# Performance work log

Measured on AMD Instinct MI355X. Metric: run time of the kernel, lower is better.

## Reference

```python
import jax, jax.numpy as jnp
import numpy as np

N_COL, N_CON, E = 100000, 20000, 800000
D_COL, D_CON, H = 16, 8, 128


def _segment_mean(msgs, dst_idx, n_dst):
    # sum then divide by in-degree (0-degree nodes get 0, matching PyG scatter-mean)
    s = jax.ops.segment_sum(msgs, dst_idx, num_segments=n_dst)
    cnt = jax.ops.segment_sum(jnp.ones((dst_idx.shape[0], 1), msgs.dtype), dst_idx, num_segments=n_dst)
    return s / jnp.maximum(cnt, 1.0)


def _sage(x_src, x_dst, src_idx, dst_idx, Wl, bl, Wr):
    # PyG SAGEConv(mean): lin_l(mean_j x_j) + lin_r(x_i); lin_r has no bias
    agg = _segment_mean(x_src[src_idx], dst_idx, x_dst.shape[0])
    return agg @ Wl.T + bl + x_dst @ Wr.T


def setup_inputs():
    key = jax.random.key(0)
    ks = jax.random.split(key, 24)
    rn = lambda k, shape, s=0.05: jax.random.normal(k, shape, jnp.float32) * s
    z = lambda shape: jnp.zeros(shape, jnp.float32)
    inp = {
        'x_col': jax.random.normal(ks[0], (N_COL, D_COL), jnp.float32),
        'x_con': jax.random.normal(ks[1], (N_CON, D_CON), jnp.float32),
        'edge_col': jax.random.randint(ks[2], (E,), 0, N_COL, jnp.int32),
        'edge_con': jax.random.randint(ks[3], (E,), 0, N_CON, jnp.int32),
        'W_col': rn(ks[4], (H, D_COL)), 'b_col': z((H,)),
        'W_con': rn(ks[5], (H, D_CON)), 'b_con': z((H,)),
        'c1_cn_Wl': rn(ks[6], (H, H)), 'c1_cn_bl': z((H,)), 'c1_cn_Wr': rn(ks[7], (H, H)),
        'c1_nc_Wl': rn(ks[8], (H, H)), 'c1_nc_bl': z((H,)), 'c1_nc_Wr': rn(ks[9], (H, H)),
        'c2_cn_Wl': rn(ks[10], (H, H)), 'c2_cn_bl': z((H,)), 'c2_cn_Wr': rn(ks[11], (H, H)),
        'c2_nc_Wl': rn(ks[12], (H, H)), 'c2_nc_bl': z((H,)), 'c2_nc_Wr': rn(ks[13], (H, H)),
        'q_W1': rn(ks[14], (H // 2, H)), 'q_b1': z((H // 2,)),
        'q_W2': rn(ks[15], (1, H // 2)), 'q_b2': z((1,)),
    }
    return inp


def reference(x_col, x_con, edge_col, edge_con,
              W_col, b_col, W_con, b_con,
              c1_cn_Wl, c1_cn_bl, c1_cn_Wr, c1_nc_Wl, c1_nc_bl, c1_nc_Wr,
              c2_cn_Wl, c2_cn_bl, c2_cn_Wr, c2_nc_Wl, c2_nc_bl, c2_nc_Wr,
              q_W1, q_b1, q_W2, q_b2):
    relu = jax.nn.relu
    h_col = relu(x_col @ W_col.T + b_col)  # [N_COL, H]
    h_con = relu(x_con @ W_con.T + b_con)  # [N_CON, H]
    # conv1: 'serves' col->con, 'served_by' con->col (reverse edges)
    n_con = relu(_sage(h_col, h_con, edge_col, edge_con, c1_cn_Wl, c1_cn_bl, c1_cn_Wr))
    n_col = relu(_sage(h_con, h_col, edge_con, edge_col, c1_nc_Wl, c1_nc_bl, c1_nc_Wr))
    # conv2
    h_con2 = relu(_sage(n_col, n_con, edge_col, edge_con, c2_cn_Wl, c2_cn_bl, c2_cn_Wr))
    h_col2 = relu(_sage(n_con, n_col, edge_con, edge_col, c2_nc_Wl, c2_nc_bl, c2_nc_Wr))
    del h_con2  # constraint embeddings unused for Q-head
    q = relu(h_col2 @ q_W1.T + q_b1) @ q_W2.T + q_b2  # [N_COL, 1]
    return q[:, 0]
```

## Files before the change

### kernel.cpp

```cpp
#include <hip/hip_runtime.h>

#define N_COL 100000
#define N_CON 20000
#define HDIM 128
#define SCAN_B 1024

__global__ void transpose_k(const float* __restrict__ src, float* __restrict__ dst, int R, int C) {
    int idx = blockIdx.x * blockDim.x + threadIdx.x;
    if (idx < R * C) {
        int r = idx / C, c = idx - r * C;
        dst[c * R + r] = src[idx];
    }
}

template <int D>
__global__ __launch_bounds__(256) void encoder_k(const float* __restrict__ x,
                                                 const float* __restrict__ WT,
                                                 const float* __restrict__ b,
                                                 float* __restrict__ out, int N) {
    int idx = blockIdx.x * blockDim.x + threadIdx.x;
    if (idx >= N * HDIM) return;
    int n = idx >> 7, h = idx & 127;
    const float* xr = x + (size_t)n * D;
    float acc = b[h];
#pragma unroll
    for (int k = 0; k < D; k++) acc = fmaf(xr[k], WT[k * HDIM + h], acc);
    out[idx] = fmaxf(acc, 0.f);
}

__global__ void count_k(const int* __restrict__ ecol, const int* __restrict__ econ,
                        int* cnt_col, int* cnt_con, int E) {
    int e = blockIdx.x * blockDim.x + threadIdx.x;
    if (e < E) {
        atomicAdd(&cnt_col[ecol[e]], 1);
        atomicAdd(&cnt_con[econ[e]], 1);
    }
}

__global__ __launch_bounds__(256) void scan1_k(const int* __restrict__ cnt, int n,
                                               int* __restrict__ offs, int* __restrict__ partials) {
    __shared__ int lds[256];
    int t = threadIdx.x;
    int base = blockIdx.x * SCAN_B + t * 4;
    int v[4], s = 0;
#pragma unroll
    for (int i = 0; i < 4; i++) { int idx = base + i; v[i] = (idx < n) ? cnt[idx] : 0; s += v[i]; }
    lds[t] = s; __syncthreads();
    for (int off = 1; off < 256; off <<= 1) {
        int x = (t >= off) ? lds[t - off] : 0; __syncthreads();
        lds[t] += x; __syncthreads();
    }
    int excl = lds[t] - s;
    if (t == 255) partials[blockIdx.x] = lds[255];
    int run = excl;
#pragma unroll
    for (int i = 0; i < 4; i++) { int idx = base + i; if (idx < n) offs[idx] = run; run += v[i]; }
}

__global__ __launch_bounds__(256) void scan2_k(int* partials, int nb) {
    __shared__ int lds[256];
    int t = threadIdx.x;
    int v = (t < nb) ? partials[t] : 0;
    lds[t] = v; __syncthreads();
    for (int off = 1; off < 256; off <<= 1) {
        int x = (t >= off) ? lds[t - off] : 0; __syncthreads();
        lds[t] += x; __syncthreads();
    }
    if (t < nb) partials[t] = lds[t] - v;
}

__global__ void scan3_k(int* offs, int n, const int* __restrict__ partials) {
    int i = blockIdx.x * blockDim.x + threadIdx.x;
    if (i < n) offs[i] += partials[i / SCAN_B];
}

__global__ void fill_k(const int* __restrict__ sidx, const int* __restrict__ didx,
                       const int* __restrict__ offs, int* cursor, int* __restrict__ srclist, int E) {
    int e = blockIdx.x * blockDim.x + threadIdx.x;
    if (e < E) {
        int d = didx[e];
        int p = offs[d] + atomicAdd(&cursor[d], 1);
        srclist[p] = sidx[e];
    }
}

__global__ __launch_bounds__(256) void gather_mean_k(const float* __restrict__ tab,
                                                     const int* __restrict__ srclist,
                                                     const int* __restrict__ offs,
                                                     const int* __restrict__ cnt,
                                                     float* __restrict__ out, int N) {
    int wid = threadIdx.x >> 6, lane = threadIdx.x & 63;
    int n = blockIdx.x * 4 + wid;
    if (n >= N) return;
    int c = cnt[n], st = offs[n];
    const int* sl = srclist + st;
    int half = lane >> 5, q = (lane & 31) * 4;
    float ax = 0.f, ay = 0.f, az = 0.f, aw = 0.f;
    int j = 0;
    for (; j + 1 < c; j += 2) {
        int s = sl[j + half];
        float4 a = *reinterpret_cast<const float4*>(tab + (size_t)s * HDIM + q);
        ax += a.x; ay += a.y; az += a.z; aw += a.w;
    }
    if (j < c && half == 0) {
        int s = sl[j];
        float4 a = *reinterpret_cast<const float4*>(tab + (size_t)s * HDIM + q);
        ax += a.x; ay += a.y; az += a.z; aw += a.w;
    }
    ax += __shfl_xor(ax, 32); ay += __shfl_xor(ay, 32);
    az += __shfl_xor(az, 32); aw += __shfl_xor(aw, 32);
    if (half == 0) {
        float inv = 1.f / fmaxf((float)c, 1.f);
        float4 r; r.x = ax * inv; r.y = ay * inv; r.z = az * inv; r.w = aw * inv;
        *reinterpret_cast<float4*>(out + (size_t)n * HDIM + q) = r;
    }
}

__device__ __forceinline__ void gemm_core(float (*As)[36], float (*Ws)[132],
                                          const float* __restrict__ src,
                                          const float* __restrict__ W,
                                          int n0, int N, int t, float acc[4][8]) {
    int tx = t & 15, ty = t >> 4;
    int ar = t >> 2, akq = (t & 3) * 8;
    int wk = t >> 3, wc = (t & 7) * 16;
    for (int kb = 0; kb < 4; ++kb) {
        int k0 = kb * 32;
        {
            int row = n0 + ar;
            float4 v0 = make_float4(0.f, 0.f, 0.f, 0.f), v1 = v0;
            if (row < N) {
                const float* ap = src + (size_t)row * HDIM + k0 + akq;
                v0 = *reinterpret_cast<const float4*>(ap);
                v1 = *reinterpret_cast<const float4*>(ap + 4);
            }
            *reinterpret_cast<float4*>(&As[ar][akq]) = v0;
            *reinterpret_cast<float4*>(&As[ar][akq + 4]) = v1;
        }
        {
            const float* wp = W + (size_t)(k0 + wk) * HDIM + wc;
#pragma unroll
            for (int jj = 0; jj < 4; jj++)
                *reinterpret_cast<float4*>(&Ws[wk][wc + 4 * jj]) =
                    *reinterpret_cast<const float4*>(wp + 4 * jj);
        }
        __syncthreads();
#pragma unroll
        for (int k4 = 0; k4 < 8; ++k4) {
            float4 av[4];
#pragma unroll
            for (int i = 0; i < 4; i++)
                av[i] = *reinterpret_cast<const float4*>(&As[ty * 4 + i][k4 * 4]);
#pragma unroll
            for (int kk = 0; kk < 4; kk++) {
                float4 w0 = *reinterpret_cast<const float4*>(&Ws[k4 * 4 + kk][tx * 4]);
                float4 w1 = *reinterpret_cast<const float4*>(&Ws[k4 * 4 + kk][64 + tx * 4]);
                float w[8] = {w0.x, w0.y, w0.z, w0.w, w1.x, w1.y, w1.z, w1.w};
#pragma unroll
                for (int i = 0; i < 4; i++) {
                    float avk = (kk == 0) ? av[i].x : (kk == 1) ? av[i].y
                                : (kk == 2) ? av[i].z : av[i].w;
#pragma unroll
                    for (int j = 0; j < 8; j++) acc[i][j] = fmaf(avk, w[j], acc[i][j]);
                }
            }
        }
        __syncthreads();
    }
}

__global__ __launch_bounds__(256) void lin_k(const float* __restrict__ src,
                                             const float* __restrict__ WT,
                                             float* __restrict__ out, int N) {
    __shared__ __align__(16) float As[64][36];
    __shared__ __align__(16) float Ws[32][132];
    int t = threadIdx.x;
    int tx = t & 15, ty = t >> 4;
    int n0 = blockIdx.x * 64;
    float acc[4][8];
#pragma unroll
    for (int i = 0; i < 4; i++)
#pragma unroll
        for (int j = 0; j < 8; j++) acc[i][j] = 0.f;
    gemm_core(As, Ws, src, WT, n0, N, t, acc);
#pragma unroll
    for (int i = 0; i < 4; i++) {
        int row = n0 + ty * 4 + i;
        if (row < N) {
            float* op = out + (size_t)row * HDIM;
            *reinterpret_cast<float4*>(op + tx * 4) = make_float4(acc[i][0], acc[i][1], acc[i][2], acc[i][3]);
            *reinterpret_cast<float4*>(op + 64 + tx * 4) = make_float4(acc[i][4], acc[i][5], acc[i][6], acc[i][7]);
        }
    }
}

__global__ __launch_bounds__(256) void sage_gemm_k(const float* __restrict__ agg,
                                                   const float* __restrict__ xdst,
                                                   const float* __restrict__ WlT,
                                                   const float* __restrict__ bl,
                                                   const float* __restrict__ WrT,
                                                   float* __restrict__ out, int N) {
    __shared__ __align__(16) float As[64][36];
    __shared__ __align__(16) float Ws[32][132];
    int t = threadIdx.x;
    int tx = t & 15, ty = t >> 4;
    int n0 = blockIdx.x * 64;
    float acc[4][8];
#pragma unroll
    for (int i = 0; i < 4; i++)
#pragma unroll
        for (int j = 0; j < 8; j++) acc[i][j] = 0.f;
    gemm_core(As, Ws, agg, WlT, n0, N, t, acc);
    gemm_core(As, Ws, xdst, WrT, n0, N, t, acc);
    float4 b0 = *reinterpret_cast<const float4*>(bl + tx * 4);
    float4 b1 = *reinterpret_cast<const float4*>(bl + 64 + tx * 4);
    float bb[8] = {b0.x, b0.y, b0.z, b0.w, b1.x, b1.y, b1.z, b1.w};
#pragma unroll
    for (int i = 0; i < 4; i++) {
        int row = n0 + ty * 4 + i;
        if (row < N) {
            float4 r0, r1;
            r0.x = fmaxf(acc[i][0] + bb[0], 0.f);
            r0.y = fmaxf(acc[i][1] + bb[1], 0.f);
            r0.z = fmaxf(acc[i][2] + bb[2], 0.f);
            r0.w = fmaxf(acc[i][3] + bb[3], 0.f);
            r1.x = fmaxf(acc[i][4] + bb[4], 0.f);
            r1.y = fmaxf(acc[i][5] + bb[5], 0.f);
            r1.z = fmaxf(acc[i][6] + bb[6], 0.f);
            r1.w = fmaxf(acc[i][7] + bb[7], 0.f);
            float* op = out + (size_t)row * HDIM;
            *reinterpret_cast<float4*>(op + tx * 4) = r0;
            *reinterpret_cast<float4*>(op + 64 + tx * 4) = r1;
        }
    }
}

__global__ __launch_bounds__(256) void sage_add_k(const float* __restrict__ c0,
                                                  const float* __restrict__ xdst,
                                                  const float* __restrict__ WrT,
                                                  const float* __restrict__ bl,
                                                  float* __restrict__ out, int N) {
    __shared__ __align__(16) float As[64][36];
    __shared__ __align__(16) float Ws[32][132];
    int t = threadIdx.x;
    int tx = t & 15, ty = t >> 4;
    int n0 = blockIdx.x * 64;
    float acc[4][8];
#pragma unroll
    for (int i = 0; i < 4; i++)
#pragma unroll
        for (int j = 0; j < 8; j++) acc[i][j] = 0.f;
    gemm_core(As, Ws, xdst, WrT, n0, N, t, acc);
    float4 b0 = *reinterpret_cast<const float4*>(bl + tx * 4);
    float4 b1 = *reinterpret_cast<const float4*>(bl + 64 + tx * 4);
    float bb[8] = {b0.x, b0.y, b0.z, b0.w, b1.x, b1.y, b1.z, b1.w};
#pragma unroll
    for (int i = 0; i < 4; i++) {
        int row = n0 + ty * 4 + i;
        if (row < N) {
            const float* cp = c0 + (size_t)row * HDIM;
            float4 c0a = *reinterpret_cast<const float4*>(cp + tx * 4);
            float4 c0b = *reinterpret_cast<const float4*>(cp + 64 + tx * 4);
            float4 r0, r1;
            r0.x = fmaxf(acc[i][0] + c0a.x + bb[0], 0.f);
            r0.y = fmaxf(acc[i][1] + c0a.y + bb[1], 0.f);
            r0.z = fmaxf(acc[i][2] + c0a.z + bb[2], 0.f);
            r0.w = fmaxf(acc[i][3] + c0a.w + bb[3], 0.f);
            r1.x = fmaxf(acc[i][4] + c0b.x + bb[4], 0.f);
            r1.y = fmaxf(acc[i][5] + c0b.y + bb[5], 0.f);
            r1.z = fmaxf(acc[i][6] + c0b.z + bb[6], 0.f);
            r1.w = fmaxf(acc[i][7] + c0b.w + bb[7], 0.f);
            float* op = out + (size_t)row * HDIM;
            *reinterpret_cast<float4*>(op + tx * 4) = r0;
            *reinterpret_cast<float4*>(op + 64 + tx * 4) = r1;
        }
    }
}

__global__ __launch_bounds__(256) void sage_add_q_k(const float* __restrict__ c0,
                                                    const float* __restrict__ xdst,
                                                    const float* __restrict__ WrT,
                                                    const float* __restrict__ bl,
                                                    const float* __restrict__ W1T,
                                                    const float* __restrict__ b1v,
                                                    const float* __restrict__ W2,
                                                    const float* __restrict__ b2,
                                                    float* __restrict__ out, int N) {
    __shared__ __align__(16) char smem[33792];
    float (*As)[36] = reinterpret_cast<float(*)[36]>(smem);
    float (*Ws)[132] = reinterpret_cast<float(*)[132]>(smem + 9216);
    float (*H2)[132] = reinterpret_cast<float(*)[132]>(smem);
    int t = threadIdx.x;
    int tx = t & 15, ty = t >> 4;
    int n0 = blockIdx.x * 64;
    float acc[4][8];
#pragma unroll
    for (int i = 0; i < 4; i++)
#pragma unroll
        for (int j = 0; j < 8; j++) acc[i][j] = 0.f;
    gemm_core(As, Ws, xdst, WrT, n0, N, t, acc);
    {
        float4 b0 = *reinterpret_cast<const float4*>(bl + tx * 4);
        float4 b1 = *reinterpret_cast<const float4*>(bl + 64 + tx * 4);
        float bb[8] = {b0.x, b0.y, b0.z, b0.w, b1.x, b1.y, b1.z, b1.w};
#pragma unroll
        for (int i = 0; i < 4; i++) {
            int row = n0 + ty * 4 + i;
            float4 c0a = make_float4(0.f, 0.f, 0.f, 0.f), c0b = c0a;
            if (row < N) {
                const float* cp = c0 + (size_t)row * HDIM;
                c0a = *reinterpret_cast<const float4*>(cp + tx * 4);
                c0b = *reinterpret_cast<const float4*>(cp + 64 + tx * 4);
            }
            float4 r0, r1;
            r0.x = fmaxf(acc[i][0] + c0a.x + bb[0], 0.f);
            r0.y = fmaxf(acc[i][1] + c0a.y + bb[1], 0.f);
            r0.z = fmaxf(acc[i][2] + c0a.z + bb[2], 0.f);
            r0.w = fmaxf(acc[i][3] + c0a.w + bb[3], 0.f);
            r1.x = fmaxf(acc[i][4] + c0b.x + bb[4], 0.f);
            r1.y = fmaxf(acc[i][5] + c0b.y + bb[5], 0.f);
            r1.z = fmaxf(acc[i][6] + c0b.z + bb[6], 0.f);
            r1.w = fmaxf(acc[i][7] + c0b.w + bb[7], 0.f);
            float* hp = &H2[ty * 4 + i][0];
            *reinterpret_cast<float4*>(hp + tx * 4) = r0;
            *reinterpret_cast<float4*>(hp + 64 + tx * 4) = r1;
        }
    }
    __syncthreads();
    int tx2 = t & 7, ty2 = t >> 3;
    float acc2[2][8];
#pragma unroll
    for (int i = 0; i < 2; i++)
#pragma unroll
        for (int j = 0; j < 8; j++) acc2[i][j] = 0.f;
    for (int k4 = 0; k4 < HDIM / 4; ++k4) {
        float4 a0 = *reinterpret_cast<const float4*>(&H2[ty2 * 2 + 0][k4 * 4]);
        float4 a1 = *reinterpret_cast<const float4*>(&H2[ty2 * 2 + 1][k4 * 4]);
        float a[2][4] = {{a0.x, a0.y, a0.z, a0.w}, {a1.x, a1.y, a1.z, a1.w}};
#pragma unroll
        for (int kk = 0; kk < 4; kk++) {
            const float* wp = W1T + (size_t)(k4 * 4 + kk) * 64 + tx2 * 8;
            float4 w0 = *reinterpret_cast<const float4*>(wp);
            float4 w1 = *reinterpret_cast<const float4*>(wp + 4);
            float w[8] = {w0.x, w0.y, w0.z, w0.w, w1.x, w1.y, w1.z, w1.w};
#pragma unroll
            for (int i = 0; i < 2; i++)
#pragma unroll
                for (int j = 0; j < 8; j++) acc2[i][j] = fmaf(a[i][kk], w[j], acc2[i][j]);
        }
    }
    {
        float4 c0v = *reinterpret_cast<const float4*>(b1v + tx2 * 8);
        float4 c1v = *reinterpret_cast<const float4*>(b1v + tx2 * 8 + 4);
        float bb1[8] = {c0v.x, c0v.y, c0v.z, c0v.w, c1v.x, c1v.y, c1v.z, c1v.w};
        float4 d0 = *reinterpret_cast<const float4*>(W2 + tx2 * 8);
        float4 d1 = *reinterpret_cast<const float4*>(W2 + tx2 * 8 + 4);
        float w2[8] = {d0.x, d0.y, d0.z, d0.w, d1.x, d1.y, d1.z, d1.w};
#pragma unroll
        for (int i = 0; i < 2; i++) {
            float v = 0.f;
#pragma unroll
            for (int j = 0; j < 8; j++) v = fmaf(fmaxf(acc2[i][j] + bb1[j], 0.f), w2[j], v);
            v += __shfl_xor(v, 1);
            v += __shfl_xor(v, 2);
            v += __shfl_xor(v, 4);
            int row = n0 + ty2 * 2 + i;
            if (tx2 == 0 && row < N) out[row] = v + b2[0];
        }
    }
}

extern "C" void kernel_launch(void* const* d_in, const int* in_sizes, int n_in,
                              void* d_out, int out_size, void* d_ws, size_t ws_size,
                              hipStream_t stream) {
    const float* x_col = (const float*)d_in[0];
    const float* x_con = (const float*)d_in[1];
    const int* edge_col = (const int*)d_in[2];
    const int* edge_con = (const int*)d_in[3];
    const float* W_col = (const float*)d_in[4];
    const float* b_col = (const float*)d_in[5];
    const float* W_con = (const float*)d_in[6];
    const float* b_con = (const float*)d_in[7];
    const float* c1_cn_Wl = (const float*)d_in[8];
    const float* c1_cn_bl = (const float*)d_in[9];
    const float* c1_cn_Wr = (const float*)d_in[10];
    const float* c1_nc_Wl = (const float*)d_in[11];
    const float* c1_nc_bl = (const float*)d_in[12];
    const float* c1_nc_Wr = (const float*)d_in[13];
    const float* c2_nc_Wl = (const float*)d_in[17];
    const float* c2_nc_bl = (const float*)d_in[18];
    const float* c2_nc_Wr = (const float*)d_in[19];
    const float* q_W1 = (const float*)d_in[20];
    const float* q_b1 = (const float*)d_in[21];
    const float* q_W2 = (const float*)d_in[22];
    const float* q_b2 = (const float*)d_in[23];
    float* out = (float*)d_out;
    const int E = in_sizes[2];

    float* ws = (float*)d_ws;
    size_t o = 0;
    float* h_col = ws + o;   o += (size_t)N_COL * HDIM;
    float* h_con = ws + o;   o += (size_t)N_CON * HDIM;
    float* n_con = ws + o;   o += (size_t)N_CON * HDIM;
    float* n_col = ws + o;   o += (size_t)N_COL * HDIM;
    float* bufA = ws + o;    o += (size_t)N_COL * HDIM;
    float* bufB = ws + o;    o += (size_t)N_CON * HDIM;
    float* W_colT = ws + o;  o += 16 * HDIM;
    float* W_conT = ws + o;  o += 8 * HDIM;
    float* c1_cn_WlT = ws + o; o += HDIM * HDIM;
    float* c1_cn_WrT = ws + o; o += HDIM * HDIM;
    float* c1_nc_WlT = ws + o; o += HDIM * HDIM;
    float* c1_nc_WrT = ws + o; o += HDIM * HDIM;
    float* c2_nc_WlT = ws + o; o += HDIM * HDIM;
    float* c2_nc_WrT = ws + o; o += HDIM * HDIM;
    float* q_W1T = ws + o;     o += HDIM * 64;
    int* iws = (int*)(ws + o);
    size_t io = 0;
    int* cnt_col = iws + io;  io += N_COL;
    int* cnt_con = iws + io;  io += N_CON;
    int* offs_col = iws + io; io += N_COL;
    int* offs_con = iws + io; io += N_CON;
    int* cursor = iws + io;   io += N_COL;
    int* partials = iws + io; io += 256;
    int* srclist_col = iws + io; io += E;
    int* srclist_con = iws + io; io += E;

    auto T = [&](const float* s, float* d, int R, int C) {
        transpose_k<<<(R * C + 255) / 256, 256, 0, stream>>>(s, d, R, C);
    };
    T(W_col, W_colT, HDIM, 16);
    T(W_con, W_conT, HDIM, 8);
    T(c1_cn_Wl, c1_cn_WlT, HDIM, HDIM);
    T(c1_cn_Wr, c1_cn_WrT, HDIM, HDIM);
    T(c1_nc_Wl, c1_nc_WlT, HDIM, HDIM);
    T(c1_nc_Wr, c1_nc_WrT, HDIM, HDIM);
    T(c2_nc_Wl, c2_nc_WlT, HDIM, HDIM);
    T(c2_nc_Wr, c2_nc_WrT, HDIM, HDIM);
    T(q_W1, q_W1T, 64, HDIM);

    encoder_k<16><<<((size_t)N_COL * HDIM + 255) / 256, 256, 0, stream>>>(x_col, W_colT, b_col, h_col, N_COL);
    encoder_k<8><<<((size_t)N_CON * HDIM + 255) / 256, 256, 0, stream>>>(x_con, W_conT, b_con, h_con, N_CON);

    hipMemsetAsync(cnt_col, 0, (N_COL + N_CON) * sizeof(int), stream);
    count_k<<<(E + 255) / 256, 256, 0, stream>>>(edge_col, edge_con, cnt_col, cnt_con, E);

    int nb_col = (N_COL + SCAN_B - 1) / SCAN_B;
    int nb_con = (N_CON + SCAN_B - 1) / SCAN_B;
    scan1_k<<<nb_col, 256, 0, stream>>>(cnt_col, N_COL, offs_col, partials);
    scan2_k<<<1, 256, 0, stream>>>(partials, nb_col);
    scan3_k<<<(N_COL + 255) / 256, 256, 0, stream>>>(offs_col, N_COL, partials);
    scan1_k<<<nb_con, 256, 0, stream>>>(cnt_con, N_CON, offs_con, partials);
    scan2_k<<<1, 256, 0, stream>>>(partials, nb_con);
    scan3_k<<<(N_CON + 255) / 256, 256, 0, stream>>>(offs_con, N_CON, partials);

    hipMemsetAsync(cursor, 0, N_COL * sizeof(int), stream);
    fill_k<<<(E + 255) / 256, 256, 0, stream>>>(edge_con, edge_col, offs_col, cursor, srclist_col, E);
    hipMemsetAsync(cursor, 0, N_CON * sizeof(int), stream);
    fill_k<<<(E + 255) / 256, 256, 0, stream>>>(edge_col, edge_con, offs_con, cursor, srclist_con, E);

    gather_mean_k<<<(N_CON + 3) / 4, 256, 0, stream>>>(h_col, srclist_con, offs_con, cnt_con, bufA, N_CON);
    sage_gemm_k<<<(N_CON + 63) / 64, 256, 0, stream>>>(bufA, h_con, c1_cn_WlT, c1_cn_bl, c1_cn_WrT, n_con, N_CON);

    lin_k<<<(N_CON + 63) / 64, 256, 0, stream>>>(h_con, c1_nc_WlT, bufB, N_CON);
    gather_mean_k<<<(N_COL + 3) / 4, 256, 0, stream>>>(bufB, srclist_col, offs_col, cnt_col, bufA, N_COL);
    sage_add_k<<<(N_COL + 63) / 64, 256, 0, stream>>>(bufA, h_col, c1_nc_WrT, c1_nc_bl, n_col, N_COL);

    lin_k<<<(N_CON + 63) / 64, 256, 0, stream>>>(n_con, c2_nc_WlT, bufB, N_CON);
    gather_mean_k<<<(N_COL + 3) / 4, 256, 0, stream>>>(bufB, srclist_col, offs_col, cnt_col, bufA, N_COL);
    sage_add_q_k<<<(N_COL + 63) / 64, 256, 0, stream>>>(bufA, n_col, c2_nc_WrT, c2_nc_bl,
                                                        q_W1T, q_b1, q_W2, q_b2, out, N_COL);
}
```

Measured before the change: 743.3 us.

## Fuse both column SAGE layers and Q-head into one kernel keeping n_col in LDS

Both neighbour aggregations for column nodes now run before a single fused kernel. That kernel computes the conv1 column output tile, keeps it in shared memory, then applies the conv2 root-weight GEMM and the Q-head MLP on it. This is possible because the conv2 neighbour term depends only on n_con. It removes the global write and read of the 100000x128 n_col tensor and one kernel launch. In exchange, shared memory per block grows to about 59 KB, which may reduce occupancy, and the two aggregate buffers are kept in memory at the same time.

Result: slower. 763.1 us (+2.7%).

```diff
diff --git a/kernel.cpp b/kernel.cpp
--- a/kernel.cpp
+++ b/kernel.cpp
@@ -168,6 +168,45 @@
     }
 }
 
+__device__ __forceinline__ void gemm_core_h(float (*Ha)[132], float (*Ws)[132],
+                                            const float* __restrict__ W,
+                                            int t, float acc[4][8]) {
+    int tx = t & 15, ty = t >> 4;
+    int wk = t >> 3, wc = (t & 7) * 16;
+    for (int kb = 0; kb < 4; ++kb) {
+        int k0 = kb * 32;
+        {
+            const float* wp = W + (size_t)(k0 + wk) * HDIM + wc;
+#pragma unroll
+            for (int jj = 0; jj < 4; jj++)
+                *reinterpret_cast<float4*>(&Ws[wk][wc + 4 * jj]) =
+                    *reinterpret_cast<const float4*>(wp + 4 * jj);
+        }
+        __syncthreads();
+#pragma unroll
+        for (int k4 = 0; k4 < 8; ++k4) {
+            float4 av[4];
+#pragma unroll
+            for (int i = 0; i < 4; i++)
+                av[i] = *reinterpret_cast<const float4*>(&Ha[ty * 4 + i][k0 + k4 * 4]);
+#pragma unroll
+            for (int kk = 0; kk < 4; kk++) {
+                float4 w0 = *reinterpret_cast<const float4*>(&Ws[k4 * 4 + kk][tx * 4]);
+                float4 w1 = *reinterpret_cast<const float4*>(&Ws[k4 * 4 + kk][64 + tx * 4]);
+                float w[8] = {w0.x, w0.y, w0.z, w0.w, w1.x, w1.y, w1.z, w1.w};
+#pragma unroll
+                for (int i = 0; i < 4; i++) {
+                    float avk = (kk == 0) ? av[i].x : (kk == 1) ? av[i].y
+                                : (kk == 2) ? av[i].z : av[i].w;
+#pragma unroll
+                    for (int j = 0; j < 8; j++) acc[i][j] = fmaf(avk, w[j], acc[i][j]);
+                }
+            }
+        }
+        __syncthreads();
+    }
+}
+
 __global__ __launch_bounds__(256) void lin_k(const float* __restrict__ src,
                                              const float* __restrict__ WT,
                                              float* __restrict__ out, int N) {
@@ -234,13 +273,22 @@
     }
 }
 
-__global__ __launch_bounds__(256) void sage_add_k(const float* __restrict__ c0,
+__global__ __launch_bounds__(256) void col_mega_k(const float* __restrict__ c0_1,
+                                                  const float* __restrict__ c0_2,
                                                   const float* __restrict__ xdst,
-                                                  const float* __restrict__ WrT,
-                                                  const float* __restrict__ bl,
+                                                  const float* __restrict__ Wr1T,
+                                                  const float* __restrict__ bl1,
+                                                  const float* __restrict__ Wr2T,
+                                                  const float* __restrict__ bl2,
+                                                  const float* __restrict__ W1T,
+                                                  const float* __restrict__ b1v,
+                                                  const float* __restrict__ W2,
+                                                  const float* __restrict__ b2,
                                                   float* __restrict__ out, int N) {
-    __shared__ __align__(16) float As[64][36];
-    __shared__ __align__(16) float Ws[32][132];
+    __shared__ __align__(16) char smem[59904];
+    float (*H)[132] = reinterpret_cast<float(*)[132]>(smem);
+    float (*As)[36] = reinterpret_cast<float(*)[36]>(smem + 33792);
+    float (*Ws)[132] = reinterpret_cast<float(*)[132]>(smem + 43008);
     int t = threadIdx.x;
     int tx = t & 15, ty = t >> 4;
     int n0 = blockIdx.x * 64;
@@ -249,83 +297,61 @@
     for (int i = 0; i < 4; i++)
 #pragma unroll
         for (int j = 0; j < 8; j++) acc[i][j] = 0.f;
-    gemm_core(As, Ws, xdst, WrT, n0, N, t, acc);
-    float4 b0 = *reinterpret_cast<const float4*>(bl + tx * 4);
-    float4 b1 = *reinterpret_cast<const float4*>(bl + 64 + tx * 4);
-    float bb[8] = {b0.x, b0.y, b0.z, b0.w, b1.x, b1.y, b1.z, b1.w};
-#pragma unroll
-    for (int i = 0; i < 4; i++) {
-        int row = n0 + ty * 4 + i;
-        if (row < N) {
-            const float* cp = c0 + (size_t)row * HDIM;
-            float4 c0a = *reinterpret_cast<const float4*>(cp + tx * 4);
-            float4 c0b = *reinterpret_cast<const float4*>(cp + 64 + tx * 4);
-            float4 r0, r1;
-            r0.x = fmaxf(acc[i][0] + c0a.x + bb[0], 0.f);
-            r0.y = fmaxf(acc[i][1] + c0a.y + bb[1], 0.f);
-            r0.z = fmaxf(acc[i][2] + c0a.z + bb[2], 0.f);
-            r0.w = fmaxf(acc[i][3] + c0a.w + bb[3], 0.f);
-            r1.x = fmaxf(acc[i][4] + c0b.x + bb[4], 0.f);
-            r1.y = fmaxf(acc[i][5] + c0b.y + bb[5], 0.f);
-            r1.z = fmaxf(acc[i][6] + c0b.z + bb[6], 0.f);
-            r1.w = fmaxf(acc[i][7] + c0b.w + bb[7], 0.f);
-            float* op = out + (size_t)row * HDIM;
-            *reinterpret_cast<float4*>(op + tx * 4) = r0;
-            *reinterpret_cast<float4*>(op + 64 + tx * 4) = r1;
-        }
-    }
-}
-
-__global__ __launch_bounds__(256) void sage_add_q_k(const float* __restrict__ c0,
-                                                    const float* __restrict__ xdst,
-                                                    const float* __restrict__ WrT,
-                                                    const float* __restrict__ bl,
-                                                    const float* __restrict__ W1T,
-                                                    const float* __restrict__ b1v,
-                                                    const float* __restrict__ W2,
-                                                    const float* __restrict__ b2,
-                                                    float* __restrict__ out, int N) {
-    __shared__ __align__(16) char smem[33792];
-    float (*As)[36] = reinterpret_cast<float(*)[36]>(smem);
-    float (*Ws)[132] = reinterpret_cast<float(*)[132]>(smem + 9216);
-    float (*H2)[132] = reinterpret_cast<float(*)[132]>(smem);
-    int t = threadIdx.x;
-    int tx = t & 15, ty = t >> 4;
-    int n0 = blockIdx.x * 64;
-    float acc[4][8];
-#pragma unroll
-    for (int i = 0; i < 4; i++)
-#pragma unroll
-        for (int j = 0; j < 8; j++) acc[i][j] = 0.f;
-    gemm_core(As, Ws, xdst, WrT, n0, N, t, acc);
+
+    gemm_core(As, Ws, xdst, Wr1T, n0, N, t, acc);
     {
-        float4 b0 = *reinterpret_cast<const float4*>(bl + tx * 4);
-        float4 b1 = *reinterpret_cast<const float4*>(bl + 64 + tx * 4);
+        float4 b0 = *reinterpret_cast<const float4*>(bl1 + tx * 4);
+        float4 b1 = *reinterpret_cast<const float4*>(bl1 + 64 + tx * 4);
         float bb[8] = {b0.x, b0.y, b0.z, b0.w, b1.x, b1.y, b1.z, b1.w};
 #pragma unroll
         for (int i = 0; i < 4; i++) {
             int row = n0 + ty * 4 + i;
-            float4 c0a = make_float4(0.f, 0.f, 0.f, 0.f), c0b = c0a;
+            float4 ca = make_float4(0.f, 0.f, 0.f, 0.f), cb = ca;
             if (row < N) {
-                const float* cp = c0 + (size_t)row * HDIM;
-                c0a = *reinterpret_cast<const float4*>(cp + tx * 4);
-                c0b = *reinterpret_cast<const float4*>(cp + 64 + tx * 4);
+                const float* cp = c0_1 + (size_t)row * HDIM;
+                ca = *reinterpret_cast<const float4*>(cp + tx * 4);
+                cb = *reinterpret_cast<const float4*>(cp + 64 + tx * 4);
             }
-            float4 r0, r1;
-            r0.x = fmaxf(acc[i][0] + c0a.x + bb[0], 0.f);
-            r0.y = fmaxf(acc[i][1] + c0a.y + bb[1], 0.f);
-            r0.z = fmaxf(acc[i][2] + c0a.z + bb[2], 0.f);
-            r0.w = fmaxf(acc[i][3] + c0a.w + bb[3], 0.f);
-            r1.x = fmaxf(acc[i][4] + c0b.x + bb[4], 0.f);
-            r1.y = fmaxf(acc[i][5] + c0b.y + bb[5], 0.f);
-            r1.z = fmaxf(acc[i][6] + c0b.z + bb[6], 0.f);
-            r1.w = fmaxf(acc[i][7] + c0b.w + bb[7], 0.f);
-            float* hp = &H2[ty * 4 + i][0];
-            *reinterpret_cast<float4*>(hp + tx * 4) = r0;
-            *reinterpret_cast<float4*>(hp + 64 + tx * 4) = r1;
+            float* hp = &H[ty * 4 + i][0];
+            *reinterpret_cast<float4*>(hp + tx * 4) = make_float4(
+                fmaxf(acc[i][0] + ca.x + bb[0], 0.f), fmaxf(acc[i][1] + ca.y + bb[1], 0.f),
+                fmaxf(acc[i][2] + ca.z + bb[2], 0.f), fmaxf(acc[i][3] + ca.w + bb[3], 0.f));
+            *reinterpret_cast<float4*>(hp + 64 + tx * 4) = make_float4(
+                fmaxf(acc[i][4] + cb.x + bb[4], 0.f), fmaxf(acc[i][5] + cb.y + bb[5], 0.f),
+                fmaxf(acc[i][6] + cb.z + bb[6], 0.f), fmaxf(acc[i][7] + cb.w + bb[7], 0.f));
         }
     }
     __syncthreads();
+
+#pragma unroll
+    for (int i = 0; i < 4; i++)
+#pragma unroll
+        for (int j = 0; j < 8; j++) acc[i][j] = 0.f;
+    gemm_core_h(H, Ws, Wr2T, t, acc);
+    {
+        float4 b0 = *reinterpret_cast<const float4*>(bl2 + tx * 4);
+        float4 b1 = *reinterpret_cast<const float4*>(bl2 + 64 + tx * 4);
+        float bb[8] = {b0.x, b0.y, b0.z, b0.w, b1.x, b1.y, b1.z, b1.w};
+#pragma unroll
+        for (int i = 0; i < 4; i++) {
+            int row = n0 + ty * 4 + i;
+            float4 ca = make_float4(0.f, 0.f, 0.f, 0.f), cb = ca;
+            if (row < N) {
+                const float* cp = c0_2 + (size_t)row * HDIM;
+                ca = *reinterpret_cast<const float4*>(cp + tx * 4);
+                cb = *reinterpret_cast<const float4*>(cp + 64 + tx * 4);
+            }
+            float* hp = &H[ty * 4 + i][0];
+            *reinterpret_cast<float4*>(hp + tx * 4) = make_float4(
+                fmaxf(acc[i][0] + ca.x + bb[0], 0.f), fmaxf(acc[i][1] + ca.y + bb[1], 0.f),
+                fmaxf(acc[i][2] + ca.z + bb[2], 0.f), fmaxf(acc[i][3] + ca.w + bb[3], 0.f));
+            *reinterpret_cast<float4*>(hp + 64 + tx * 4) = make_float4(
+                fmaxf(acc[i][4] + cb.x + bb[4], 0.f), fmaxf(acc[i][5] + cb.y + bb[5], 0.f),
+                fmaxf(acc[i][6] + cb.z + bb[6], 0.f), fmaxf(acc[i][7] + cb.w + bb[7], 0.f));
+        }
+    }
+    __syncthreads();
+
     int tx2 = t & 7, ty2 = t >> 3;
     float acc2[2][8];
 #pragma unroll
@@ -333,8 +359,8 @@
 #pragma unroll
         for (int j = 0; j < 8; j++) acc2[i][j] = 0.f;
     for (int k4 = 0; k4 < HDIM / 4; ++k4) {
-        float4 a0 = *reinterpret_cast<const float4*>(&H2[ty2 * 2 + 0][k4 * 4]);
-        float4 a1 = *reinterpret_cast<const float4*>(&H2[ty2 * 2 + 1][k4 * 4]);
+        float4 a0 = *reinterpret_cast<const float4*>(&H[ty2 * 2 + 0][k4 * 4]);
+        float4 a1 = *reinterpret_cast<const float4*>(&H[ty2 * 2 + 1][k4 * 4]);
         float a[2][4] = {{a0.x, a0.y, a0.z, a0.w}, {a1.x, a1.y, a1.z, a1.w}};
 #pragma unroll
         for (int kk = 0; kk < 4; kk++) {
@@ -401,8 +427,8 @@
     float* h_col = ws + o;   o += (size_t)N_COL * HDIM;
     float* h_con = ws + o;   o += (size_t)N_CON * HDIM;
     float* n_con = ws + o;   o += (size_t)N_CON * HDIM;
-    float* n_col = ws + o;   o += (size_t)N_COL * HDIM;
-    float* bufA = ws + o;    o += (size_t)N_COL * HDIM;
+    float* c01 = ws + o;     o += (size_t)N_COL * HDIM;
+    float* c02 = ws + o;     o += (size_t)N_COL * HDIM;
     float* bufB = ws + o;    o += (size_t)N_CON * HDIM;
     float* W_colT = ws + o;  o += 16 * HDIM;
     float* W_conT = ws + o;  o += 8 * HDIM;
@@ -457,15 +483,15 @@
     hipMemsetAsync(cursor, 0, N_CON * sizeof(int), stream);
     fill_k<<<(E + 255) / 256, 256, 0, stream>>>(edge_col, edge_con, offs_con, cursor, srclist_con, E);
 
-    gather_mean_k<<<(N_CON + 3) / 4, 256, 0, stream>>>(h_col, srclist_con, offs_con, cnt_con, bufA, N_CON);
-    sage_gemm_k<<<(N_CON + 63) / 64, 256, 0, stream>>>(bufA, h_con, c1_cn_WlT, c1_cn_bl, c1_cn_WrT, n_con, N_CON);
+    gather_mean_k<<<(N_CON + 3) / 4, 256, 0, stream>>>(h_col, srclist_con, offs_con, cnt_con, bufB, N_CON);
+    sage_gemm_k<<<(N_CON + 63) / 64, 256, 0, stream>>>(bufB, h_con, c1_cn_WlT, c1_cn_bl, c1_cn_WrT, n_con, N_CON);
 
     lin_k<<<(N_CON + 63) / 64, 256, 0, stream>>>(h_con, c1_nc_WlT, bufB, N_CON);
-    gather_mean_k<<<(N_COL + 3) / 4, 256, 0, stream>>>(bufB, srclist_col, offs_col, cnt_col, bufA, N_COL);
-    sage_add_k<<<(N_COL + 63) / 64, 256, 0, stream>>>(bufA, h_col, c1_nc_WrT, c1_nc_bl, n_col, N_COL);
-
+    gather_mean_k<<<(N_COL + 3) / 4, 256, 0, stream>>>(bufB, srclist_col, offs_col, cnt_col, c01, N_COL);
     lin_k<<<(N_CON + 63) / 64, 256, 0, stream>>>(n_con, c2_nc_WlT, bufB, N_CON);
-    gather_mean_k<<<(N_COL + 3) / 4, 256, 0, stream>>>(bufB, srclist_col, offs_col, cnt_col, bufA, N_COL);
-    sage_add_q_k<<<(N_COL + 63) / 64, 256, 0, stream>>>(bufA, n_col, c2_nc_WrT, c2_nc_bl,
-                                                        q_W1T, q_b1, q_W2, q_b2, out, N_COL);
-}
+    gather_mean_k<<<(N_COL + 3) / 4, 256, 0, stream>>>(bufB, srclist_col, offs_col, cnt_col, c02, N_COL);
+
+    col_mega_k<<<(N_COL + 63) / 64, 256, 0, stream>>>(c01, c02, h_col,
+                                                      c1_nc_WrT, c1_nc_bl, c2_nc_WrT, c2_nc_bl,
+                                                      q_W1T, q_b1, q_W2, q_b2, out, N_COL);
+}
```
